# Optimization experiments

Measured on AMD Instinct MI355X. Metric: run time of the kernel, lower is better.

## Reference

```python
import jax, jax.numpy as jnp
import numpy as np

HIDDEN = 64
HALF = 32
VOCAB = 64
B, L = 256, 2048


def _l2norm(x):
    # matches torch F.normalize(dim=-1, eps=1e-12)
    return x / jnp.maximum(jnp.linalg.norm(x, axis=-1, keepdims=True), 1e-12)


def setup_inputs() -> dict:
    key = jax.random.key(0)
    ks = jax.random.split(key, 16)
    s = 0.02
    return {
        "seq": jax.random.randint(ks[0], (B, L), 0, VOCAB),
        "embed": jax.random.normal(ks[1], (VOCAB, HIDDEN), jnp.float32) * s,
        "W1": jax.random.normal(ks[2], (2 * HIDDEN, HIDDEN), jnp.float32) * s,
        "b1": jnp.zeros((2 * HIDDEN,), jnp.float32),
        "W2": jax.random.normal(ks[3], (HIDDEN, 2 * HIDDEN), jnp.float32) * s,
        "b2": jnp.zeros((HIDDEN,), jnp.float32),
        "ln_g": jnp.ones((HIDDEN,), jnp.float32),
        "ln_b": jnp.zeros((HIDDEN,), jnp.float32),
        "Ws": jax.random.normal(ks[4], (HALF, HIDDEN), jnp.float32) * s,
        "bs": jnp.zeros((HALF,), jnp.float32),
        "We": jax.random.normal(ks[5], (HALF, HIDDEN), jnp.float32) * s,
        "be": jnp.zeros((HALF,), jnp.float32),
        "Wrp": jax.random.normal(ks[6], (HIDDEN, 2 * HALF), jnp.float32) * s,
        "brp": jnp.zeros((HIDDEN,), jnp.float32),
        "Wo": jax.random.normal(ks[7], (VOCAB, HIDDEN), jnp.float32) * s,
        "bo": jnp.zeros((VOCAB,), jnp.float32),
    }


def reference(seq, embed, W1, b1, W2, b2, ln_g, ln_b, Ws, bs, We, be, Wrp, brp, Wo, bo):
    # Encoder: embed -> LayerNorm(h + FF(h))
    h0 = embed[seq]                                     # [B,L,H]
    ff = jnp.maximum(h0 @ W1.T + b1, 0.0) @ W2.T + b2
    x = h0 + ff
    mu = x.mean(-1, keepdims=True)
    var = x.var(-1, keepdims=True)
    h = (x - mu) / jnp.sqrt(var + 1e-5) * ln_g + ln_b   # [B,L,H]

    Bn, Ln, _ = h.shape
    half = Ws.shape[0]
    hs_all = h @ Ws.T + bs                              # [B,L,half]
    he_all = h @ We.T + be

    # sequential delta-rule memory writes over t = 0 .. L-2
    hs_seq = jnp.swapaxes(hs_all[:, :-1], 0, 1)         # [L-1,B,half]
    he_seq = jnp.swapaxes(he_all[:, :-1], 0, 1)
    scales = (jnp.arange(1, Ln) / Ln).astype(h.dtype)   # (t+1)/L
    M0 = jnp.zeros((Bn, half, half), h.dtype)

    def step(carry, inp):
        M_s, M_e = carry
        hs, he, sc = inp
        ks_ = _l2norm(hs)
        ke_ = _l2norm(he)
        vps = jnp.einsum('bij,bj->bi', M_s, ks_)
        vpe = jnp.einsum('bij,bj->bi', M_e, ke_)
        M_s = M_s + (hs - vps)[:, :, None] * ks_[:, None, :]
        M_e = M_e + sc * (he - vpe)[:, :, None] * ke_[:, None, :]
        return (M_s, M_e), None

    (M_s, M_e), _ = jax.lax.scan(step, (M0, M0), (hs_seq, he_seq, scales))

    # read with last-position query
    qs = _l2norm(hs_all[:, -1])
    qe = _l2norm(he_all[:, -1])
    rs = jnp.einsum('bij,bj->bi', M_s, qs)
    re = jnp.einsum('bij,bj->bi', M_e, qe)
    r = jnp.concatenate([rs, re], axis=-1)              # [B, 2*half]
    return (r @ Wrp.T + brp) @ Wo.T + bo                # [B, vocab]
```

## Files before the change

### kernel.cpp

```cpp
#include <hip/hip_runtime.h>

#define HIDDEN 64
#define HALFD  32
#define VOCAB  64
#define BATCH  256
#define SEQLEN 2048

#define RLF(v, sl) __int_as_float(__builtin_amdgcn_readlane(__float_as_int(v), (sl)))
#define RLI(v, sl) __builtin_amdgcn_readlane((v), (sl))
#define GIX(j,m) (((j)==0?0:(j)==1?7:(j)==2?13:(j)==3?18:(j)==4?22:(j)==5?25:27) + (m) - (j) - 1)
#define OM(m) (((m)*((m)+1))>>1)

__global__ __launch_bounds__(64) void vocab_kernel(
    const float* __restrict__ embed, const float* __restrict__ W1, const float* __restrict__ b1,
    const float* __restrict__ W2, const float* __restrict__ b2,
    const float* __restrict__ ln_g, const float* __restrict__ ln_b,
    const float* __restrict__ Ws, const float* __restrict__ bs,
    const float* __restrict__ We, const float* __restrict__ be,
    float* __restrict__ ws)
{
    const int v = blockIdx.x;
    const int tid = threadIdx.x;

    __shared__ float e_s[64];
    __shared__ float a1_s[128];
    __shared__ float h_s[64];

    e_s[tid] = embed[v * 64 + tid];
    __syncthreads();

    float p0 = b1[tid], p1 = 0.f, p2 = 0.f, p3 = 0.f;
    float q0 = b1[tid + 64], q1 = 0.f, q2 = 0.f, q3 = 0.f;
    #pragma unroll
    for (int m = 0; m < 64; m += 4) {
        p0 = fmaf(e_s[m],   W1[tid * 64 + m],     p0);
        p1 = fmaf(e_s[m+1], W1[tid * 64 + m + 1], p1);
        p2 = fmaf(e_s[m+2], W1[tid * 64 + m + 2], p2);
        p3 = fmaf(e_s[m+3], W1[tid * 64 + m + 3], p3);
        q0 = fmaf(e_s[m],   W1[(tid + 64) * 64 + m],     q0);
        q1 = fmaf(e_s[m+1], W1[(tid + 64) * 64 + m + 1], q1);
        q2 = fmaf(e_s[m+2], W1[(tid + 64) * 64 + m + 2], q2);
        q3 = fmaf(e_s[m+3], W1[(tid + 64) * 64 + m + 3], q3);
    }
    a1_s[tid]      = fmaxf((p0 + p1) + (p2 + p3), 0.0f);
    a1_s[tid + 64] = fmaxf((q0 + q1) + (q2 + q3), 0.0f);
    __syncthreads();

    float f0 = b2[tid], f1 = 0.f, f2 = 0.f, f3 = 0.f;
    #pragma unroll
    for (int m = 0; m < 128; m += 4) {
        f0 = fmaf(a1_s[m],   W2[tid * 128 + m],     f0);
        f1 = fmaf(a1_s[m+1], W2[tid * 128 + m + 1], f1);
        f2 = fmaf(a1_s[m+2], W2[tid * 128 + m + 2], f2);
        f3 = fmaf(a1_s[m+3], W2[tid * 128 + m + 3], f3);
    }
    float x = e_s[tid] + ((f0 + f1) + (f2 + f3));

    float s = x, s2 = x * x;
    #pragma unroll
    for (int off = 32; off >= 1; off >>= 1) {
        s  += __shfl_xor(s,  off, 64);
        s2 += __shfl_xor(s2, off, 64);
    }
    float mu  = s * (1.0f / 64.0f);
    float var = s2 * (1.0f / 64.0f) - mu * mu;
    float hval = (x - mu) * rsqrtf(var + 1e-5f) * ln_g[tid] + ln_b[tid];
    h_s[tid] = hval;
    __syncthreads();

    const int j = tid & 31;
    const bool is_s = tid < 32;
    const float* W = is_s ? Ws : We;
    float c0 = is_s ? bs[j] : be[j];
    float c1 = 0.f, c2 = 0.f, c3 = 0.f;
    #pragma unroll
    for (int m = 0; m < 64; m += 4) {
        c0 = fmaf(h_s[m],   W[j * 64 + m],     c0);
        c1 = fmaf(h_s[m+1], W[j * 64 + m + 1], c1);
        c2 = fmaf(h_s[m+2], W[j * 64 + m + 2], c2);
        c3 = fmaf(h_s[m+3], W[j * 64 + m + 3], c3);
    }
    float acc = (c0 + c1) + (c2 + c3);

    float n2 = acc * acc;
    #pragma unroll
    for (int off = 16; off >= 1; off >>= 1) n2 += __shfl_xor(n2, off, 64);
    float norm = sqrtf(n2);
    float kn = acc / fmaxf(norm, 1e-12f);

    const int base = v * 32 + j;
    if (is_s) { ws[base]        = kn; ws[4096 + base] = acc; }
    else      { ws[2048 + base] = kn; ws[6144 + base] = acc; }
}

__global__ __launch_bounds__(256) void gram_kernel(float* __restrict__ ws)
{
    const int w   = blockIdx.x & 1;
    const int seg = blockIdx.x >> 1;
    const int tid = threadIdx.x;
    __shared__ float k_s[64][33];
    const float* kb = ws + w * 2048;
    for (int i = tid; i < 2048; i += 256) k_s[i >> 5][i & 31] = kb[i];
    __syncthreads();
    const int a  = seg * 16 + (tid >> 4);
    const int b0 = (tid & 15) << 2;
    float* Gw = ws + 8192 + w * 4096 + a * 64;
    #pragma unroll
    for (int bb = 0; bb < 4; ++bb) {
        const int bcol = b0 + bb;
        float acc0 = 0.f, acc1 = 0.f;
        #pragma unroll
        for (int m = 0; m < 32; m += 2) {
            acc0 = fmaf(k_s[a][m],     k_s[bcol][m],     acc0);
            acc1 = fmaf(k_s[a][m + 1], k_s[bcol][m + 1], acc1);
        }
        Gw[bcol] = acc0 + acc1;
    }
}

static __device__ __forceinline__ void build_wpack(
    const int* tj, float fb, float invL, bool is_e, bool is_last, float* Wp,
    const float* __restrict__ Gg)
{
    float f[8];
    #pragma unroll
    for (int j = 0; j < 8; ++j) f[j] = is_e ? (fb + (float)j * invL) : 1.0f;
    if (is_last) f[7] = 0.0f;

    float g[28];
    #pragma unroll
    for (int j = 0; j < 7; ++j)
        #pragma unroll
        for (int m = j + 1; m < 8; ++m) g[GIX(j, m)] = Gg[tj[j] * 64 + tj[m]];

    #pragma unroll
    for (int m = 0; m < 8; ++m) {
        float col[8];
        col[m] = f[m];
        #pragma unroll
        for (int j = 6; j >= 0; --j) {
            if (j < m) {
                float acc = 0.0f;
                #pragma unroll
                for (int p = 1; p < 8; ++p)
                    if (p > j && p <= m) acc = fmaf(g[GIX(j, p)], col[p], acc);
                col[j] = -f[j] * acc;
            }
        }
        #pragma unroll
        for (int j = 0; j < 8; ++j)
            if (j <= m) Wp[OM(m) + j] = col[j];
    }
}

struct Chunk {
    int   tokv;
    int   tk[8];
    float grow[8];
    float R[8];
    float braw;
    float bp[8];
};

__global__ __launch_bounds__(128) void scan_kernel(
    const int* __restrict__ seq, const float* __restrict__ ws,
    const float* __restrict__ Wrp, const float* __restrict__ brp,
    const float* __restrict__ Wo, const float* __restrict__ bo,
    float* __restrict__ out)
{
    const int b    = blockIdx.x;
    const int tid  = threadIdx.x;
    const int w    = tid >> 6;
    const int lane = tid & 63;
    const int l7   = lane & 7;
    const bool is_e = (w == 1);

    __shared__ __align__(16) float Wlds[2][256][8][8];
    __shared__ __align__(16) int   toklds[SEQLEN];
    __shared__ float wacc_s[2][64];
    __shared__ float r_s[64];
    __shared__ float t1_s[64];

    const float* Gg = ws + 8192 + w * 4096;
    const int*   sq = seq + b * SEQLEN;

    {
        const int4* sq4 = (const int4*)sq;
        int4* tl = (int4*)toklds;
        #pragma unroll
        for (int i = 0; i < 4; ++i) tl[tid + i * 128] = sq4[tid + i * 128];
    }
    __syncthreads();

    {
        const float invL = 1.0f / (float)SEQLEN;
        #pragma unroll
        for (int qq = 0; qq < 4; ++qq) {
            const int c = lane + (qq << 6);
            int tj[8];
            #pragma unroll
            for (int j = 0; j < 8; ++j) tj[j] = toklds[c * 8 + j];
            float Wp[36];
            build_wpack(tj, (float)(8 * c + 1) * invL, invL, is_e, c == 255, Wp, Gg);
            const int cx = c & 7;
            #pragma unroll
            for (int i = 0; i < 8; ++i) {
                float r[8];
                #pragma unroll
                for (int m = 0; m < 8; ++m) r[m] = (m >= i) ? Wp[OM(m) + i] : 0.0f;
                float4* dst = (float4*)&Wlds[w][c][i ^ cx][0];
                dst[0] = make_float4(r[0], r[1], r[2], r[3]);
                dst[1] = make_float4(r[4], r[5], r[6], r[7]);
            }
        }
    }
    __syncthreads();

    Chunk A, B;
    float u, wacc0 = 0.0f, wacc1 = 0.0f;
    float sp0, sp1, sp2, sp3, sp4, sp5, sp6, sp7;

    A.tokv = sq[2040 + l7];
    B.tokv = sq[2032 + l7];
    int tv2 = sq[2024 + l7];
    #pragma unroll
    for (int j = 0; j < 8; ++j) A.tk[j] = RLI(A.tokv, j);
    #pragma unroll
    for (int j = 0; j < 8; ++j) A.grow[j] = Gg[A.tk[j] * 64 + lane];
    {
        const float4* rp = (const float4*)&Wlds[w][255][l7 ^ 7][0];
        float4 lo = rp[0], hi = rp[1];
        A.R[0] = lo.x; A.R[1] = lo.y; A.R[2] = lo.z; A.R[3] = lo.w;
        A.R[4] = hi.x; A.R[5] = hi.y; A.R[6] = hi.z; A.R[7] = hi.w;
    }
    u = Gg[A.tk[7] * 64 + lane];
    A.braw = __shfl(u, A.tokv, 64);
    B.braw = __shfl(u, B.tokv, 64);
    #pragma unroll
    for (int j = 0; j < 8; ++j) {
        A.bp[j] = 0.0f;
        B.bp[j] = __shfl(A.grow[j], B.tokv, 64);
    }
    sp0 = sp1 = sp2 = sp3 = sp4 = sp5 = sp6 = sp7 = 0.0f;

    auto body = [&](Chunk& cur, Chunk& nxt, int c) {
        const int cm1 = (c > 0) ? c - 1 : 0;
        const int cm3 = (c > 2) ? c - 3 : 0;

        float c01 = fmaf(cur.bp[1], sp1, cur.bp[0] * sp0);
        float c23 = fmaf(cur.bp[3], sp3, cur.bp[2] * sp2);
        float c45 = fmaf(cur.bp[5], sp5, cur.bp[4] * sp4);
        float c67 = fmaf(cur.bp[7], sp7, cur.bp[6] * sp6);
        float tl = cur.braw - ((c01 + c23) + (c45 + c67));
        float t0 = RLF(tl, 0), t1 = RLF(tl, 1), t2 = RLF(tl, 2), t3 = RLF(tl, 3);
        float t4 = RLF(tl, 4), t5 = RLF(tl, 5), t6 = RLF(tl, 6), t7 = RLF(tl, 7);

        #pragma unroll
        for (int j = 0; j < 8; ++j) nxt.tk[j] = RLI(nxt.tokv, j);
        #pragma unroll
        for (int j = 0; j < 8; ++j) nxt.grow[j] = Gg[nxt.tk[j] * 64 + lane];
        {
            const float4* rp = (const float4*)&Wlds[w][cm1][l7 ^ (cm1 & 7)][0];
            float4 lo = rp[0], hi = rp[1];
            nxt.R[0] = lo.x; nxt.R[1] = lo.y; nxt.R[2] = lo.z; nxt.R[3] = lo.w;
            nxt.R[4] = hi.x; nxt.R[5] = hi.y; nxt.R[6] = hi.z; nxt.R[7] = hi.w;
        }
        int tv3 = sq[cm3 * 8 + l7];

        const float* R = cur.R;
        float a0 = fmaf(R[1], t1, R[0] * t0);
        float a1 = fmaf(R[3], t3, R[2] * t2);
        float a2 = fmaf(R[5], t5, R[4] * t4);
        float a3 = fmaf(R[7], t7, R[6] * t6);
        float sd = (a0 + a1) + (a2 + a3);
        float s0 = RLF(sd, 0), s1 = RLF(sd, 1), s2 = RLF(sd, 2), s3 = RLF(sd, 3);
        float s4 = RLF(sd, 4), s5 = RLF(sd, 5), s6 = RLF(sd, 6), s7 = RLF(sd, 7);

        float dA = fmaf(cur.grow[0], s0, fmaf(cur.grow[1], s1, fmaf(cur.grow[2], s2, cur.grow[3] * s3)));
        float dB = fmaf(cur.grow[4], s4, fmaf(cur.grow[5], s5, fmaf(cur.grow[6], s6, cur.grow[7] * s7)));
        u -= (dA + dB);
        cur.braw = __shfl(u, tv2, 64);
        #pragma unroll
        for (int j = 0; j < 8; ++j)
            nxt.bp[j] = __shfl(cur.grow[j], nxt.tokv, 64);

        wacc0 += (lane == cur.tk[0]) ? s0 : 0.0f;
        wacc1 += (lane == cur.tk[1]) ? s1 : 0.0f;
        wacc0 += (lane == cur.tk[2]) ? s2 : 0.0f;
        wacc1 += (lane == cur.tk[3]) ? s3 : 0.0f;
        wacc0 += (lane == cur.tk[4]) ? s4 : 0.0f;
        wacc1 += (lane == cur.tk[5]) ? s5 : 0.0f;
        wacc0 += (lane == cur.tk[6]) ? s6 : 0.0f;
        wacc1 += (lane == cur.tk[7]) ? s7 : 0.0f;

        cur.tokv = tv2; tv2 = tv3;
        sp0 = s0; sp1 = s1; sp2 = s2; sp3 = s3;
        sp4 = s4; sp5 = s5; sp6 = s6; sp7 = s7;
    };

    for (int c = 255; c >= 1; c -= 2) {
        body(A, B, c);
        body(B, A, c - 1);
    }

    wacc_s[w][lane] = wacc0 + wacc1;
    __syncthreads();

    if (tid < 64) {
        const int w2  = tid >> 5;
        const int rho = tid & 31;
        const float* vv = ws + 4096 + w2 * 2048;
        const float* wa = &wacc_s[w2][0];
        float acc = 0.0f;
        #pragma unroll 8
        for (int tok = 0; tok < 64; ++tok) acc = fmaf(wa[tok], vv[tok * 32 + rho], acc);
        r_s[tid] = acc;
    }
    __syncthreads();

    if (tid < 64) {
        float acc = brp[tid];
        #pragma unroll 8
        for (int m = 0; m < 64; ++m) acc = fmaf(Wrp[tid * 64 + m], r_s[m], acc);
        t1_s[tid] = acc;
    }
    __syncthreads();
    if (tid < 64) {
        float acc = bo[tid];
        #pragma unroll 8
        for (int m = 0; m < 64; ++m) acc = fmaf(Wo[tid * 64 + m], t1_s[m], acc);
        out[b * 64 + tid] = acc;
    }
}

extern "C" void kernel_launch(void* const* d_in, const int* in_sizes, int n_in,
                              void* d_out, int out_size, void* d_ws, size_t ws_size,
                              hipStream_t stream)
{
    const int*   seq   = (const int*)  d_in[0];
    const float* embed = (const float*)d_in[1];
    const float* W1    = (const float*)d_in[2];
    const float* b1    = (const float*)d_in[3];
    const float* W2    = (const float*)d_in[4];
    const float* b2    = (const float*)d_in[5];
    const float* ln_g  = (const float*)d_in[6];
    const float* ln_b  = (const float*)d_in[7];
    const float* Ws    = (const float*)d_in[8];
    const float* bs    = (const float*)d_in[9];
    const float* We    = (const float*)d_in[10];
    const float* be    = (const float*)d_in[11];
    const float* Wrp   = (const float*)d_in[12];
    const float* brp   = (const float*)d_in[13];
    const float* Wo    = (const float*)d_in[14];
    const float* bo    = (const float*)d_in[15];
    float* ws  = (float*)d_ws;
    float* out = (float*)d_out;

    hipLaunchKernelGGL(vocab_kernel, dim3(VOCAB), dim3(64), 0, stream,
                       embed, W1, b1, W2, b2, ln_g, ln_b, Ws, bs, We, be, ws);
    hipLaunchKernelGGL(gram_kernel, dim3(8), dim3(256), 0, stream, ws);
    hipLaunchKernelGGL(scan_kernel, dim3(BATCH), dim3(128), 0, stream,
                       seq, ws, Wrp, brp, Wo, bo, out);
}
```

Before: 190.6 us.

## Stage vocab weights in LDS and use ds_swizzle broadcasts in scan

The vocab kernel now runs 256 threads per block and cooperatively loads W1, W2, Ws and We into padded shared memory with float4 reads. W2 and Ws/We loading overlaps with the earlier matvec stages, replacing strided per-thread global reads. In the scan inner loop, the eight readlane broadcasts of tl and sd are replaced with ds_swizzle broadcasts, and the next-chunk bp shuffles are hoisted earlier to overlap their latency. Swizzle goes through the LDS crossbar rather than scalar registers, which may add latency on the sequential critical path.

```diff
diff --git a/kernel.cpp b/kernel.cpp
--- a/kernel.cpp
+++ b/kernel.cpp
@@ -8,10 +8,11 @@
 
 #define RLF(v, sl) __int_as_float(__builtin_amdgcn_readlane(__float_as_int(v), (sl)))
 #define RLI(v, sl) __builtin_amdgcn_readlane((v), (sl))
+#define SWZF(v, j) __int_as_float(__builtin_amdgcn_ds_swizzle(__float_as_int(v), ((j) << 5)))
 #define GIX(j,m) (((j)==0?0:(j)==1?7:(j)==2?13:(j)==3?18:(j)==4?22:(j)==5?25:27) + (m) - (j) - 1)
 #define OM(m) (((m)*((m)+1))>>1)
 
-__global__ __launch_bounds__(64) void vocab_kernel(
+__global__ __launch_bounds__(256) void vocab_kernel(
     const float* __restrict__ embed, const float* __restrict__ W1, const float* __restrict__ b1,
     const float* __restrict__ W2, const float* __restrict__ b2,
     const float* __restrict__ ln_g, const float* __restrict__ ln_b,
@@ -23,74 +24,103 @@
     const int tid = threadIdx.x;
 
     __shared__ float e_s[64];
+    __shared__ float W1_s[128][65];
+    __shared__ float W2_s[64][129];
+    __shared__ float Wse_s[64][65];
     __shared__ float a1_s[128];
     __shared__ float h_s[64];
 
-    e_s[tid] = embed[v * 64 + tid];
-    __syncthreads();
-
-    float p0 = b1[tid], p1 = 0.f, p2 = 0.f, p3 = 0.f;
-    float q0 = b1[tid + 64], q1 = 0.f, q2 = 0.f, q3 = 0.f;
-    #pragma unroll
-    for (int m = 0; m < 64; m += 4) {
-        p0 = fmaf(e_s[m],   W1[tid * 64 + m],     p0);
-        p1 = fmaf(e_s[m+1], W1[tid * 64 + m + 1], p1);
-        p2 = fmaf(e_s[m+2], W1[tid * 64 + m + 2], p2);
-        p3 = fmaf(e_s[m+3], W1[tid * 64 + m + 3], p3);
-        q0 = fmaf(e_s[m],   W1[(tid + 64) * 64 + m],     q0);
-        q1 = fmaf(e_s[m+1], W1[(tid + 64) * 64 + m + 1], q1);
-        q2 = fmaf(e_s[m+2], W1[(tid + 64) * 64 + m + 2], q2);
-        q3 = fmaf(e_s[m+3], W1[(tid + 64) * 64 + m + 3], q3);
-    }
-    a1_s[tid]      = fmaxf((p0 + p1) + (p2 + p3), 0.0f);
-    a1_s[tid + 64] = fmaxf((q0 + q1) + (q2 + q3), 0.0f);
-    __syncthreads();
-
-    float f0 = b2[tid], f1 = 0.f, f2 = 0.f, f3 = 0.f;
-    #pragma unroll
-    for (int m = 0; m < 128; m += 4) {
-        f0 = fmaf(a1_s[m],   W2[tid * 128 + m],     f0);
-        f1 = fmaf(a1_s[m+1], W2[tid * 128 + m + 1], f1);
-        f2 = fmaf(a1_s[m+2], W2[tid * 128 + m + 2], f2);
-        f3 = fmaf(a1_s[m+3], W2[tid * 128 + m + 3], f3);
-    }
-    float x = e_s[tid] + ((f0 + f1) + (f2 + f3));
-
-    float s = x, s2 = x * x;
-    #pragma unroll
-    for (int off = 32; off >= 1; off >>= 1) {
-        s  += __shfl_xor(s,  off, 64);
-        s2 += __shfl_xor(s2, off, 64);
-    }
-    float mu  = s * (1.0f / 64.0f);
-    float var = s2 * (1.0f / 64.0f) - mu * mu;
-    float hval = (x - mu) * rsqrtf(var + 1e-5f) * ln_g[tid] + ln_b[tid];
-    h_s[tid] = hval;
-    __syncthreads();
-
-    const int j = tid & 31;
-    const bool is_s = tid < 32;
-    const float* W = is_s ? Ws : We;
-    float c0 = is_s ? bs[j] : be[j];
-    float c1 = 0.f, c2 = 0.f, c3 = 0.f;
-    #pragma unroll
-    for (int m = 0; m < 64; m += 4) {
-        c0 = fmaf(h_s[m],   W[j * 64 + m],     c0);
-        c1 = fmaf(h_s[m+1], W[j * 64 + m + 1], c1);
-        c2 = fmaf(h_s[m+2], W[j * 64 + m + 2], c2);
-        c3 = fmaf(h_s[m+3], W[j * 64 + m + 3], c3);
-    }
-    float acc = (c0 + c1) + (c2 + c3);
-
-    float n2 = acc * acc;
-    #pragma unroll
-    for (int off = 16; off >= 1; off >>= 1) n2 += __shfl_xor(n2, off, 64);
-    float norm = sqrtf(n2);
-    float kn = acc / fmaxf(norm, 1e-12f);
-
-    const int base = v * 32 + j;
-    if (is_s) { ws[base]        = kn; ws[4096 + base] = acc; }
-    else      { ws[2048 + base] = kn; ws[6144 + base] = acc; }
+    if (tid < 64) e_s[tid] = embed[v * 64 + tid];
+    {
+        const float4* src = (const float4*)W1;
+        for (int i = tid; i < 2048; i += 256) {
+            float4 x4 = src[i];
+            const int e = i << 2, r = e >> 6, c = e & 63;
+            W1_s[r][c] = x4.x; W1_s[r][c+1] = x4.y; W1_s[r][c+2] = x4.z; W1_s[r][c+3] = x4.w;
+        }
+    }
+    __syncthreads();
+
+    if (tid < 128) {
+        float p0 = b1[tid], p1 = 0.f, p2 = 0.f, p3 = 0.f;
+        #pragma unroll
+        for (int m = 0; m < 64; m += 4) {
+            p0 = fmaf(e_s[m],   W1_s[tid][m],   p0);
+            p1 = fmaf(e_s[m+1], W1_s[tid][m+1], p1);
+            p2 = fmaf(e_s[m+2], W1_s[tid][m+2], p2);
+            p3 = fmaf(e_s[m+3], W1_s[tid][m+3], p3);
+        }
+        a1_s[tid] = fmaxf((p0 + p1) + (p2 + p3), 0.0f);
+    } else {
+        const float4* src = (const float4*)W2;
+        for (int i = tid - 128; i < 2048; i += 128) {
+            float4 x4 = src[i];
+            const int e = i << 2, r = e >> 7, c = e & 127;
+            W2_s[r][c] = x4.x; W2_s[r][c+1] = x4.y; W2_s[r][c+2] = x4.z; W2_s[r][c+3] = x4.w;
+        }
+    }
+    __syncthreads();
+
+    if (tid < 64) {
+        float f0 = b2[tid], f1 = 0.f, f2 = 0.f, f3 = 0.f;
+        #pragma unroll
+        for (int m = 0; m < 128; m += 4) {
+            f0 = fmaf(a1_s[m],   W2_s[tid][m],   f0);
+            f1 = fmaf(a1_s[m+1], W2_s[tid][m+1], f1);
+            f2 = fmaf(a1_s[m+2], W2_s[tid][m+2], f2);
+            f3 = fmaf(a1_s[m+3], W2_s[tid][m+3], f3);
+        }
+        float x = e_s[tid] + ((f0 + f1) + (f2 + f3));
+        float s = x, s2 = x * x;
+        #pragma unroll
+        for (int off = 32; off >= 1; off >>= 1) {
+            s  += __shfl_xor(s,  off, 64);
+            s2 += __shfl_xor(s2, off, 64);
+        }
+        float mu  = s * (1.0f / 64.0f);
+        float var = s2 * (1.0f / 64.0f) - mu * mu;
+        h_s[tid] = (x - mu) * rsqrtf(var + 1e-5f) * ln_g[tid] + ln_b[tid];
+    } else if (tid < 192) {
+        const int t2 = tid - 64;
+        const float4* s1 = (const float4*)Ws;
+        const float4* s2 = (const float4*)We;
+        for (int i = t2; i < 512; i += 128) {
+            float4 x4 = s1[i];
+            const int e = i << 2, r = e >> 6, c = e & 63;
+            Wse_s[r][c] = x4.x; Wse_s[r][c+1] = x4.y; Wse_s[r][c+2] = x4.z; Wse_s[r][c+3] = x4.w;
+        }
+        for (int i = t2; i < 512; i += 128) {
+            float4 x4 = s2[i];
+            const int e = i << 2, r = e >> 6, c = e & 63;
+            Wse_s[32+r][c] = x4.x; Wse_s[32+r][c+1] = x4.y; Wse_s[32+r][c+2] = x4.z; Wse_s[32+r][c+3] = x4.w;
+        }
+    }
+    __syncthreads();
+
+    if (tid < 64) {
+        const int j = tid & 31;
+        const bool is_s = tid < 32;
+        float c0 = is_s ? bs[j] : be[j];
+        float c1 = 0.f, c2 = 0.f, c3 = 0.f;
+        #pragma unroll
+        for (int m = 0; m < 64; m += 4) {
+            c0 = fmaf(h_s[m],   Wse_s[tid][m],   c0);
+            c1 = fmaf(h_s[m+1], Wse_s[tid][m+1], c1);
+            c2 = fmaf(h_s[m+2], Wse_s[tid][m+2], c2);
+            c3 = fmaf(h_s[m+3], Wse_s[tid][m+3], c3);
+        }
+        float acc = (c0 + c1) + (c2 + c3);
+
+        float n2 = acc * acc;
+        #pragma unroll
+        for (int off = 16; off >= 1; off >>= 1) n2 += __shfl_xor(n2, off, 64);
+        float norm = sqrtf(n2);
+        float kn = acc / fmaxf(norm, 1e-12f);
+
+        const int base = v * 32 + j;
+        if (is_s) { ws[base]        = kn; ws[4096 + base] = acc; }
+        else      { ws[2048 + base] = kn; ws[6144 + base] = acc; }
+    }
 }
 
 __global__ __launch_bounds__(256) void gram_kernel(float* __restrict__ ws)
@@ -252,9 +282,12 @@
         float c45 = fmaf(cur.bp[5], sp5, cur.bp[4] * sp4);
         float c67 = fmaf(cur.bp[7], sp7, cur.bp[6] * sp6);
         float tl = cur.braw - ((c01 + c23) + (c45 + c67));
-        float t0 = RLF(tl, 0), t1 = RLF(tl, 1), t2 = RLF(tl, 2), t3 = RLF(tl, 3);
-        float t4 = RLF(tl, 4), t5 = RLF(tl, 5), t6 = RLF(tl, 6), t7 = RLF(tl, 7);
-
+
+        float t0 = SWZF(tl, 0), t1 = SWZF(tl, 1), t2 = SWZF(tl, 2), t3 = SWZF(tl, 3);
+        float t4 = SWZF(tl, 4), t5 = SWZF(tl, 5), t6 = SWZF(tl, 6), t7 = SWZF(tl, 7);
+
+        #pragma unroll
+        for (int j = 0; j < 8; ++j) nxt.bp[j] = __shfl(cur.grow[j], nxt.tokv, 64);
         #pragma unroll
         for (int j = 0; j < 8; ++j) nxt.tk[j] = RLI(nxt.tokv, j);
         #pragma unroll
@@ -273,16 +306,14 @@
         float a2 = fmaf(R[5], t5, R[4] * t4);
         float a3 = fmaf(R[7], t7, R[6] * t6);
         float sd = (a0 + a1) + (a2 + a3);
-        float s0 = RLF(sd, 0), s1 = RLF(sd, 1), s2 = RLF(sd, 2), s3 = RLF(sd, 3);
-        float s4 = RLF(sd, 4), s5 = RLF(sd, 5), s6 = RLF(sd, 6), s7 = RLF(sd, 7);
+
+        float s0 = SWZF(sd, 0), s1 = SWZF(sd, 1), s2 = SWZF(sd, 2), s3 = SWZF(sd, 3);
+        float s4 = SWZF(sd, 4), s5 = SWZF(sd, 5), s6 = SWZF(sd, 6), s7 = SWZF(sd, 7);
 
         float dA = fmaf(cur.grow[0], s0, fmaf(cur.grow[1], s1, fmaf(cur.grow[2], s2, cur.grow[3] * s3)));
         float dB = fmaf(cur.grow[4], s4, fmaf(cur.grow[5], s5, fmaf(cur.grow[6], s6, cur.grow[7] * s7)));
         u -= (dA + dB);
         cur.braw = __shfl(u, tv2, 64);
-        #pragma unroll
-        for (int j = 0; j < 8; ++j)
-            nxt.bp[j] = __shfl(cur.grow[j], nxt.tokv, 64);
 
         wacc0 += (lane == cur.tk[0]) ? s0 : 0.0f;
         wacc1 += (lane == cur.tk[1]) ? s1 : 0.0f;
@@ -356,7 +387,7 @@
     float* ws  = (float*)d_ws;
     float* out = (float*)d_out;
 
-    hipLaunchKernelGGL(vocab_kernel, dim3(VOCAB), dim3(64), 0, stream,
+    hipLaunchKernelGGL(vocab_kernel, dim3(VOCAB), dim3(256), 0, stream,
                        embed, W1, b1, W2, b2, ln_g, ln_b, Ws, bs, We, be, ws);
     hipLaunchKernelGGL(gram_kernel, dim3(8), dim3(256), 0, stream, ws);
     hipLaunchKernelGGL(scan_kernel, dim3(BATCH), dim3(128), 0, stream,
```

Result: no change. 193.7 us (+1.6%).
